# Kernel tuning notes

Hardware: AMD Instinct MI355X
Metric: run time of the kernel (lower is better)

## Reference

```python
import jax, jax.numpy as jnp
import numpy as np

TEMPERATURE = 0.1
NEG_INF = -1e30


def setup_inputs() -> dict:
    key = jax.random.key(0)
    kf, kl = jax.random.split(key)
    N, D = 8192, 128
    features = jax.random.normal(kf, (N, D), dtype=jnp.float32)
    # labels in [-1, 80): -1 marks background rows that are filtered out
    labels = jax.random.randint(kl, (N,), -1, 80)
    return {"features": features, "labels": labels}


def reference(features, labels):
    N = labels.shape[0]
    fg = labels >= 0  # [N]

    # F.normalize(p=2, dim=1): x / max(||x||, eps)
    norm = jnp.maximum(jnp.linalg.norm(features, axis=1, keepdims=True), 1e-12)
    f = features / norm

    sim = jnp.matmul(f, f.T) / TEMPERATURE  # [N, N]

    pair_fg = fg[:, None] & fg[None, :]
    eye = jnp.eye(N, dtype=bool)
    label_eq = labels[:, None] == labels[None, :]
    pos_mask = pair_fg & label_eq & ~eye          # positives (same label, not self)
    all_mask = pair_fg & ~eye                     # pos | neg == everything but self (within fg)

    # row-wise masked max, clamped to [-20, 20] as in the original
    max_sim = jnp.max(jnp.where(all_mask, sim, NEG_INF), axis=1)
    max_sim = jnp.clip(max_sim, -20.0, 20.0)

    e = jnp.exp(sim - max_sim[:, None])           # cos-sim/temp is bounded, no overflow
    pos_sum = jnp.clip(jnp.sum(jnp.where(pos_mask, e, 0.0), axis=1), 1e-6, 1e6)
    all_sum = jnp.clip(jnp.sum(jnp.where(all_mask, e, 0.0), axis=1), 1e-6, 1e6)

    loss_i = jnp.minimum(-jnp.log(pos_sum / all_sum), 10.0)  # clamp(max=10)

    # rows contributing to the mean: fg rows with at least one positive
    valid = fg & (jnp.sum(pos_mask, axis=1) > 0)
    n_valid = jnp.sum(valid)
    mean_loss = jnp.sum(jnp.where(valid, loss_i, 0.0)) / jnp.maximum(n_valid, 1).astype(jnp.float32)

    ok = (jnp.sum(fg) >= 2) & (n_valid > 0)
    return jnp.where(ok, mean_loss, jnp.float32(0.0))
```

## Files before the change

### kernel.cpp

```cpp
#include <hip/hip_runtime.h>

#define N 8192
#define D 128
#define CHUNK 512
#define NCHUNK (N / CHUNK)
#define TILE_IT (CHUNK / 128)

typedef unsigned short u16;
typedef __attribute__((ext_vector_type(8))) __bf16 bf16x8;
typedef __attribute__((ext_vector_type(4))) float f32x4;

#define PREP_SCALE 3.7982889979f

__device__ __forceinline__ u16 f2bf(float x) {
  unsigned u = __float_as_uint(x);
  u += 0x7fff + ((u >> 16) & 1);
  return (u16)(u >> 16);
}
__device__ __forceinline__ float bf2f(u16 h) {
  return __uint_as_float(((unsigned)h) << 16);
}

__global__ __launch_bounds__(256) void cpe_prep(const float* __restrict__ feat,
                                                u16* __restrict__ fhi,
                                                u16* __restrict__ flo,
                                                float* __restrict__ acc3) {
  if (blockIdx.x == 0 && threadIdx.x < 4) acc3[threadIdx.x] = 0.0f;
  const int w = threadIdx.x >> 6, l = threadIdx.x & 63;
  const int row = blockIdx.x * 4 + w;
  const float2 x = *(const float2*)&feat[row * D + l * 2];
  float s = x.x * x.x + x.y * x.y;
#pragma unroll
  for (int sh = 1; sh < 64; sh <<= 1) s += __shfl_xor(s, sh);
  const float inv = PREP_SCALE / fmaxf(sqrtf(s), 1e-12f);
  const float a = x.x * inv, b = x.y * inv;
  const u16 ah = f2bf(a), bh = f2bf(b);
  const u16 al = f2bf(a - bf2f(ah)), bl = f2bf(b - bf2f(bh));
  *(ushort2*)&fhi[row * D + l * 2] = make_ushort2(ah, bh);
  *(ushort2*)&flo[row * D + l * 2] = make_ushort2(al, bl);
}

__global__ __launch_bounds__(256, 2) void cpe_main(
    const u16* __restrict__ fhi, const u16* __restrict__ flo,
    const int* __restrict__ labels, float4* __restrict__ partials) {
  __shared__ __align__(16) u16 Bh[128 * 128];
  __shared__ __align__(16) u16 Bl[128 * 128];
  __shared__ int Lab[CHUNK];
  const int rt = blockIdx.x, cc = blockIdx.y;
  const int tid = threadIdx.x;
  const int w = tid >> 6, l = tid & 63, q = l >> 4, m = l & 15;
  const int r0w = rt * 256 + w * 64;
  const int cbase0 = cc * CHUNK;

  Lab[tid] = labels[cbase0 + tid];
  Lab[tid + 256] = labels[cbase0 + 256 + tid];

  bf16x8 Ah[4][4];
  int labi[4][4];
#pragma unroll
  for (int tr = 0; tr < 4; ++tr) {
    const int row = r0w + tr * 16 + m;
#pragma unroll
    for (int ks = 0; ks < 4; ++ks)
      Ah[tr][ks] = *(const bf16x8*)&fhi[row * D + ks * 32 + q * 8];
#pragma unroll
    for (int v = 0; v < 4; ++v) labi[tr][v] = labels[r0w + tr * 16 + q * 4 + v];
  }

  float mxe[4][4], ps[4][4], as_[4][4];
#pragma unroll
  for (int tr = 0; tr < 4; ++tr)
#pragma unroll
    for (int v = 0; v < 4; ++v) { mxe[tr][v] = 0.f; ps[tr][v] = 0.f; as_[tr][v] = 0.f; }

  for (int it = 0; it < TILE_IT; ++it) {
    const int cbase = cbase0 + it * 128;
    __syncthreads();
#pragma unroll
    for (int n = 0; n < 8; ++n) {
      const int r = w * 32 + n * 4 + q;
      const int c = m ^ (r & 15);
      const u16* gh = &fhi[(size_t)(cbase + r) * D + c * 8];
      const u16* gl = &flo[(size_t)(cbase + r) * D + c * 8];
      __builtin_amdgcn_global_load_lds(
          (const __attribute__((address_space(1))) unsigned*)gh,
          (__attribute__((address_space(3))) unsigned*)&Bh[(w * 512 + n * 64) * 8],
          16, 0, 0);
      __builtin_amdgcn_global_load_lds(
          (const __attribute__((address_space(1))) unsigned*)gl,
          (__attribute__((address_space(3))) unsigned*)&Bl[(w * 512 + n * 64) * 8],
          16, 0, 0);
    }
    __syncthreads();

    for (int ct = 0; ct < 8; ++ct) {
      const int jj = ct * 16 + m;
      f32x4 acc[4];
#pragma unroll
      for (int tr = 0; tr < 4; ++tr) acc[tr] = (f32x4){0.f, 0.f, 0.f, 0.f};
#pragma unroll
      for (int ks = 0; ks < 4; ++ks) {
        const int off = jj * 128 + ((ks * 4 + q) ^ m) * 8;
        const bf16x8 bh = *(const bf16x8*)&Bh[off];
        const bf16x8 bl = *(const bf16x8*)&Bl[off];
#pragma unroll
        for (int tr = 0; tr < 4; ++tr)
          acc[tr] = __builtin_amdgcn_mfma_f32_16x16x32_bf16(Ah[tr][ks], bh, acc[tr], 0, 0, 0);
#pragma unroll
        for (int tr = 0; tr < 4; ++tr)
          acc[tr] = __builtin_amdgcn_mfma_f32_16x16x32_bf16(Ah[tr][ks], bl, acc[tr], 0, 0, 0);
      }
      const int labj = Lab[it * 128 + jj];
      const bool fgj = labj >= 0;
      const int jbase = cbase + ct * 16;
#pragma unroll
      for (int tr = 0; tr < 4; ++tr) {
        if (jbase == r0w + tr * 16) {
#pragma unroll
          for (int v = 0; v < 4; ++v) {
            const float e = exp2f(acc[tr][v]);
            const float em = (fgj && (m != q * 4 + v)) ? e : 0.0f;
            as_[tr][v] += em;
            mxe[tr][v] = fmaxf(mxe[tr][v], em);
            ps[tr][v] += (labj == labi[tr][v]) ? em : 0.0f;
          }
        } else {
#pragma unroll
          for (int v = 0; v < 4; ++v) {
            const float e = exp2f(acc[tr][v]);
            const float em = fgj ? e : 0.0f;
            as_[tr][v] += em;
            mxe[tr][v] = fmaxf(mxe[tr][v], em);
            ps[tr][v] += (labj == labi[tr][v]) ? em : 0.0f;
          }
        }
      }
    }
  }

#pragma unroll
  for (int tr = 0; tr < 4; ++tr)
#pragma unroll
    for (int v = 0; v < 4; ++v) {
      float vm = mxe[tr][v], vp = ps[tr][v], va = as_[tr][v];
#pragma unroll
      for (int s = 1; s < 16; s <<= 1) {
        vm = fmaxf(vm, __shfl_xor(vm, s));
        vp += __shfl_xor(vp, s);
        va += __shfl_xor(va, s);
      }
      if (m == 0)
        partials[(size_t)cc * N + r0w + tr * 16 + q * 4 + v] =
            make_float4(vm, vp, va, 0.f);
    }
}

__global__ __launch_bounds__(256) void cpe_rows(const float4* __restrict__ partials,
                                                const int* __restrict__ labels,
                                                float* __restrict__ acc3,
                                                float* __restrict__ out) {
  const int r = blockIdx.x * 256 + threadIdx.x;
  float mxe = 0.f, ps = 0.f, as_ = 0.f;
#pragma unroll
  for (int c = 0; c < NCHUNK; ++c) {
    const float4 p = partials[(size_t)c * N + r];
    mxe = fmaxf(mxe, p.x); ps += p.y; as_ += p.z;
  }
  const bool fg = labels[r] >= 0;
  const bool valid = fg && (ps > 0.f);
  const float pos = fminf(fmaxf(ps / mxe, 1e-6f), 1e6f);
  const float all = fminf(fmaxf(as_ / mxe, 1e-6f), 1e6f);
  const float loss = fminf(-logf(pos / all), 10.0f);
  float v0 = valid ? loss : 0.f;
  float v1 = valid ? 1.f : 0.f;
  float v2 = fg ? 1.f : 0.f;
#pragma unroll
  for (int s = 1; s < 64; s <<= 1) {
    v0 += __shfl_xor(v0, s); v1 += __shfl_xor(v1, s); v2 += __shfl_xor(v2, s);
  }
  __shared__ float red[3][4];
  const int w = threadIdx.x >> 6, l = threadIdx.x & 63;
  if (l == 0) { red[0][w] = v0; red[1][w] = v1; red[2][w] = v2; }
  __syncthreads();
  if (threadIdx.x == 0) {
    atomicAdd(&acc3[0], red[0][0] + red[0][1] + red[0][2] + red[0][3]);
    atomicAdd(&acc3[1], red[1][0] + red[1][1] + red[1][2] + red[1][3]);
    atomicAdd(&acc3[2], red[2][0] + red[2][1] + red[2][2] + red[2][3]);
    __threadfence();
    const unsigned old = atomicAdd((unsigned*)&acc3[3], 1u);
    if (old == gridDim.x - 1) {
      const float ls = atomicAdd(&acc3[0], 0.0f);
      const float nv = atomicAdd(&acc3[1], 0.0f);
      const float nf = atomicAdd(&acc3[2], 0.0f);
      out[0] = (nf >= 2.0f && nv > 0.0f) ? ls / fmaxf(nv, 1.0f) : 0.0f;
    }
  }
}

extern "C" void kernel_launch(void* const* d_in, const int* in_sizes, int n_in,
                              void* d_out, int out_size, void* d_ws, size_t ws_size,
                              hipStream_t stream) {
  const float* feat = (const float*)d_in[0];
  const int* labels = (const int*)d_in[1];
  float* out = (float*)d_out;
  char* ws = (char*)d_ws;
  u16* fhi = (u16*)ws;
  u16* flo = (u16*)(ws + (size_t)N * D * 2);
  float4* partials = (float4*)(ws + (size_t)N * D * 4);
  float* acc3 = (float*)(ws + (size_t)N * D * 4 + (size_t)NCHUNK * N * 16);

  cpe_prep<<<N / 4, 256, 0, stream>>>(feat, fhi, flo, acc3);
  cpe_main<<<dim3(N / 256, NCHUNK), 256, 0, stream>>>(fhi, flo, labels, partials);
  cpe_rows<<<N / 256, 256, 0, stream>>>(partials, labels, acc3, out);
}
```

Baseline: 116.6 us.

## Sort rows by label to skip background tiles and simplify off-label epilogue

Adds a single-block counting sort of rows by label and permutes the normalized features into sorted order. The main kernel then skips 16-column tiles that are entirely background, avoiding both their MFMAs and their exp work. For tiles whose label range cannot overlap the row block's labels or the diagonal, it uses a cheaper epilogue with no mask or positive-label checks. It also switches to the raw hardware exp2 intrinsic, at the cost of an extra serial sort kernel launch.

```diff
diff --git a/kernel.cpp b/kernel.cpp
--- a/kernel.cpp
+++ b/kernel.cpp
@@ -5,6 +5,7 @@
 #define CHUNK 512
 #define NCHUNK (N / CHUNK)
 #define TILE_IT (CHUNK / 128)
+#define NBIN 81
 
 typedef unsigned short u16;
 typedef __attribute__((ext_vector_type(8))) __bf16 bf16x8;
@@ -21,13 +22,38 @@
   return __uint_as_float(((unsigned)h) << 16);
 }
 
+__global__ __launch_bounds__(256) void cpe_sort(const int* __restrict__ labels,
+                                                int* __restrict__ perm,
+                                                int* __restrict__ slab,
+                                                float* __restrict__ acc3) {
+  __shared__ int hist[NBIN];
+  __shared__ int base[NBIN];
+  const int t = threadIdx.x;
+  if (t < NBIN) hist[t] = 0;
+  if (t < 4) acc3[t] = 0.0f;
+  __syncthreads();
+  for (int i = t; i < N; i += 256) atomicAdd(&hist[labels[i] + 1], 1);
+  __syncthreads();
+  if (t == 0) {
+    int s = 0;
+    for (int b = 0; b < NBIN; ++b) { base[b] = s; s += hist[b]; }
+  }
+  __syncthreads();
+  for (int i = t; i < N; i += 256) {
+    const int lab = labels[i];
+    const int pos = atomicAdd(&base[lab + 1], 1);
+    perm[pos] = i;
+    slab[pos] = lab;
+  }
+}
+
 __global__ __launch_bounds__(256) void cpe_prep(const float* __restrict__ feat,
+                                                const int* __restrict__ perm,
                                                 u16* __restrict__ fhi,
-                                                u16* __restrict__ flo,
-                                                float* __restrict__ acc3) {
-  if (blockIdx.x == 0 && threadIdx.x < 4) acc3[threadIdx.x] = 0.0f;
+                                                u16* __restrict__ flo) {
   const int w = threadIdx.x >> 6, l = threadIdx.x & 63;
-  const int row = blockIdx.x * 4 + w;
+  const int srow = blockIdx.x * 4 + w;
+  const int row = perm[srow];
   const float2 x = *(const float2*)&feat[row * D + l * 2];
   float s = x.x * x.x + x.y * x.y;
 #pragma unroll
@@ -36,13 +62,13 @@
   const float a = x.x * inv, b = x.y * inv;
   const u16 ah = f2bf(a), bh = f2bf(b);
   const u16 al = f2bf(a - bf2f(ah)), bl = f2bf(b - bf2f(bh));
-  *(ushort2*)&fhi[row * D + l * 2] = make_ushort2(ah, bh);
-  *(ushort2*)&flo[row * D + l * 2] = make_ushort2(al, bl);
+  *(ushort2*)&fhi[srow * D + l * 2] = make_ushort2(ah, bh);
+  *(ushort2*)&flo[srow * D + l * 2] = make_ushort2(al, bl);
 }
 
 __global__ __launch_bounds__(256, 2) void cpe_main(
     const u16* __restrict__ fhi, const u16* __restrict__ flo,
-    const int* __restrict__ labels, float4* __restrict__ partials) {
+    const int* __restrict__ slab, float4* __restrict__ partials) {
   __shared__ __align__(16) u16 Bh[128 * 128];
   __shared__ __align__(16) u16 Bl[128 * 128];
   __shared__ int Lab[CHUNK];
@@ -52,8 +78,10 @@
   const int r0w = rt * 256 + w * 64;
   const int cbase0 = cc * CHUNK;
 
-  Lab[tid] = labels[cbase0 + tid];
-  Lab[tid + 256] = labels[cbase0 + 256 + tid];
+  Lab[tid] = slab[cbase0 + tid];
+  Lab[tid + 256] = slab[cbase0 + 256 + tid];
+
+  const int labi_lo = slab[r0w], labi_hi = slab[r0w + 63];
 
   bf16x8 Ah[4][4];
   int labi[4][4];
@@ -64,7 +92,7 @@
     for (int ks = 0; ks < 4; ++ks)
       Ah[tr][ks] = *(const bf16x8*)&fhi[row * D + ks * 32 + q * 8];
 #pragma unroll
-    for (int v = 0; v < 4; ++v) labi[tr][v] = labels[r0w + tr * 16 + q * 4 + v];
+    for (int v = 0; v < 4; ++v) labi[tr][v] = slab[r0w + tr * 16 + q * 4 + v];
   }
 
   float mxe[4][4], ps[4][4], as_[4][4];
@@ -94,6 +122,10 @@
     __syncthreads();
 
     for (int ct = 0; ct < 8; ++ct) {
+      const int tb = it * 128 + ct * 16;
+      const int labj_lo = Lab[tb], labj_hi = Lab[tb + 15];
+      if (labj_hi < 0) continue;
+      const bool slow = (labj_lo < 0) | ((labj_hi >= labi_lo) & (labj_lo <= labi_hi));
       const int jj = ct * 16 + m;
       f32x4 acc[4];
 #pragma unroll
@@ -110,28 +142,39 @@
         for (int tr = 0; tr < 4; ++tr)
           acc[tr] = __builtin_amdgcn_mfma_f32_16x16x32_bf16(Ah[tr][ks], bl, acc[tr], 0, 0, 0);
       }
-      const int labj = Lab[it * 128 + jj];
-      const bool fgj = labj >= 0;
-      const int jbase = cbase + ct * 16;
-#pragma unroll
-      for (int tr = 0; tr < 4; ++tr) {
-        if (jbase == r0w + tr * 16) {
+      if (!slow) {
+#pragma unroll
+        for (int tr = 0; tr < 4; ++tr)
 #pragma unroll
           for (int v = 0; v < 4; ++v) {
-            const float e = exp2f(acc[tr][v]);
-            const float em = (fgj && (m != q * 4 + v)) ? e : 0.0f;
-            as_[tr][v] += em;
-            mxe[tr][v] = fmaxf(mxe[tr][v], em);
-            ps[tr][v] += (labj == labi[tr][v]) ? em : 0.0f;
+            const float e = __builtin_amdgcn_exp2f(acc[tr][v]);
+            as_[tr][v] += e;
+            mxe[tr][v] = fmaxf(mxe[tr][v], e);
           }
-        } else {
-#pragma unroll
-          for (int v = 0; v < 4; ++v) {
-            const float e = exp2f(acc[tr][v]);
-            const float em = fgj ? e : 0.0f;
-            as_[tr][v] += em;
-            mxe[tr][v] = fmaxf(mxe[tr][v], em);
-            ps[tr][v] += (labj == labi[tr][v]) ? em : 0.0f;
+      } else {
+        const int labj = Lab[tb + m];
+        const bool fgj = labj >= 0;
+        const int jbase = cbase + ct * 16;
+#pragma unroll
+        for (int tr = 0; tr < 4; ++tr) {
+          if (jbase == r0w + tr * 16) {
+#pragma unroll
+            for (int v = 0; v < 4; ++v) {
+              const float e = __builtin_amdgcn_exp2f(acc[tr][v]);
+              const float em = (fgj && (m != q * 4 + v)) ? e : 0.0f;
+              as_[tr][v] += em;
+              mxe[tr][v] = fmaxf(mxe[tr][v], em);
+              ps[tr][v] += (labj == labi[tr][v]) ? em : 0.0f;
+            }
+          } else {
+#pragma unroll
+            for (int v = 0; v < 4; ++v) {
+              const float e = __builtin_amdgcn_exp2f(acc[tr][v]);
+              const float em = fgj ? e : 0.0f;
+              as_[tr][v] += em;
+              mxe[tr][v] = fmaxf(mxe[tr][v], em);
+              ps[tr][v] += (labj == labi[tr][v]) ? em : 0.0f;
+            }
           }
         }
       }
@@ -156,7 +199,7 @@
 }
 
 __global__ __launch_bounds__(256) void cpe_rows(const float4* __restrict__ partials,
-                                                const int* __restrict__ labels,
+                                                const int* __restrict__ slab,
                                                 float* __restrict__ acc3,
                                                 float* __restrict__ out) {
   const int r = blockIdx.x * 256 + threadIdx.x;
@@ -166,7 +209,7 @@
     const float4 p = partials[(size_t)c * N + r];
     mxe = fmaxf(mxe, p.x); ps += p.y; as_ += p.z;
   }
-  const bool fg = labels[r] >= 0;
+  const bool fg = slab[r] >= 0;
   const bool valid = fg && (ps > 0.f);
   const float pos = fminf(fmaxf(ps / mxe, 1e-6f), 1e6f);
   const float all = fminf(fmaxf(as_ / mxe, 1e-6f), 1e6f);
@@ -208,8 +251,11 @@
   u16* flo = (u16*)(ws + (size_t)N * D * 2);
   float4* partials = (float4*)(ws + (size_t)N * D * 4);
   float* acc3 = (float*)(ws + (size_t)N * D * 4 + (size_t)NCHUNK * N * 16);
-
-  cpe_prep<<<N / 4, 256, 0, stream>>>(feat, fhi, flo, acc3);
-  cpe_main<<<dim3(N / 256, NCHUNK), 256, 0, stream>>>(fhi, flo, labels, partials);
-  cpe_rows<<<N / 256, 256, 0, stream>>>(partials, labels, acc3, out);
-}
+  int* perm = (int*)(ws + (size_t)N * D * 4 + (size_t)NCHUNK * N * 16 + 256);
+  int* slab = perm + N;
+
+  cpe_sort<<<1, 256, 0, stream>>>(labels, perm, slab, acc3);
+  cpe_prep<<<N / 4, 256, 0, stream>>>(feat, perm, fhi, flo);
+  cpe_main<<<dim3(N / 256, NCHUNK), 256, 0, stream>>>(fhi, flo, slab, partials);
+  cpe_rows<<<N / 256, 256, 0, stream>>>(partials, slab, acc3, out);
+}
```

Measured after the change: 125.8 us. +7.9%, slower.
